# Performance work log

Measured on AMD Instinct MI355X. Metric: run time of the kernel, lower is better.

## Reference

```python
import jax, jax.numpy as jnp
import numpy as np

N_NODES = 50000
N_EDGES = 600000
D = 128
DROP_P = 0.5


def setup_inputs() -> dict:
    key = jax.random.key(0)
    k1, k2, k3, k4, k5, k6 = jax.random.split(key, 6)
    x = jax.random.normal(k1, (N_NODES, D), dtype=jnp.float32)
    W = jax.random.normal(k2, (D, D), dtype=jnp.float32) * (1.0 / np.sqrt(D))
    b = jax.random.normal(k3, (D,), dtype=jnp.float32) * 0.01
    mask_u = jax.random.uniform(k4, (N_NODES, D), dtype=jnp.float32)
    src = jax.random.randint(k5, (N_EDGES,), 0, N_NODES, dtype=jnp.int64)
    dst = jax.random.randint(k6, (N_EDGES,), 0, N_NODES, dtype=jnp.int64)
    return {"x": x, "W": W, "b": b, "mask_u": mask_u, "src": src, "dst": dst}


def reference(x, W, b, mask_u, src, dst):
    n_nodes = x.shape[0]
    # linear + relu (nn.Linear stores weight as [out, in]; here W is [out, in])
    h = jax.nn.relu(jnp.einsum('nd,od->no', x, W) + b)
    # inverted dropout with precomputed uniform noise (train mode, p=0.5)
    keep = (mask_u >= DROP_P).astype(h.dtype)
    h = h * keep * (1.0 / (1.0 - DROP_P))
    # message passing: msg = h[src], reduce = sum over incoming edges per dst
    msgs = jnp.take(h, src, axis=0)            # [E, D] gather
    out = jax.ops.segment_sum(msgs, dst, num_segments=n_nodes)  # [N, D]
    return out
```

## Files before the change

kernel.cpp:

```cpp
#include <hip/hip_runtime.h>

#define D 128
#define TILE_N 32
#define HPITCH 132
#define CAP 48
#define SPILL_MAX 8192

typedef __attribute__((ext_vector_type(8))) short  short8;
typedef __attribute__((ext_vector_type(4))) float  f32x4;

__device__ inline unsigned short f32_to_bf16(float f) {
    unsigned int u = __float_as_uint(f);
    unsigned int r = (u + 0x7FFFu + ((u >> 16) & 1u)) >> 16;
    return (unsigned short)r;
}
__device__ inline float bf16_to_f32(unsigned short s) {
    return __uint_as_float(((unsigned int)s) << 16);
}
__device__ inline short8 pack_bf16x8(float4 a, float4 b) {
    short8 u;
    u[0] = (short)f32_to_bf16(a.x); u[1] = (short)f32_to_bf16(a.y);
    u[2] = (short)f32_to_bf16(a.z); u[3] = (short)f32_to_bf16(a.w);
    u[4] = (short)f32_to_bf16(b.x); u[5] = (short)f32_to_bf16(b.y);
    u[6] = (short)f32_to_bf16(b.z); u[7] = (short)f32_to_bf16(b.w);
    return u;
}

__global__ __launch_bounds__(256) void prep_kernel(
    const float* __restrict__ W, unsigned short* __restrict__ Wb,
    int* __restrict__ cnt, int n_nodes, int* __restrict__ spill_cnt)
{
    const int tid = blockIdx.x * 256 + threadIdx.x;
    if (tid < (D * D) / 8) {
        float4 v0 = *(const float4*)&W[tid * 8];
        float4 v1 = *(const float4*)&W[tid * 8 + 4];
        *(short8*)&Wb[tid * 8] = pack_bf16x8(v0, v1);
    }
    if (cnt && tid < n_nodes) cnt[tid] = 0;
    if (spill_cnt && tid == 0) *spill_cnt = 0;
}

__global__ __launch_bounds__(256, 8) void gemm_mfma_kernel(
    const float* __restrict__ x, const unsigned short* __restrict__ Wb,
    const float* __restrict__ bias, const float* __restrict__ mask_u,
    unsigned short* __restrict__ h, int n_nodes,
    const int* __restrict__ src, const int* __restrict__ dst, int n_edges,
    int* __restrict__ cnt, int* __restrict__ bucket,
    int* __restrict__ spill_cnt, int* __restrict__ spill)
{
    __shared__ unsigned short ht[TILE_N * HPITCH];
    const int t    = threadIdx.x;
    const int lane = t & 63;
    const int w    = t >> 6;
    const int ws   = w >> 1;
    const int cs   = w & 1;
    const int fr   = lane & 15;
    const int fg   = lane >> 4;

    const int n0 = blockIdx.x * TILE_N;

    const int e0 = blockIdx.x * 256 + t;
    int e_dst = 0, e_src = 0;
    const bool has_e0 = (e0 < n_edges);
    if (has_e0) { e_dst = dst[e0]; e_src = src[e0]; }

    int arow = n0 + 16 * ws + fr;
    if (arow >= n_nodes) arow = n_nodes - 1;
    const float* xrow = x + (size_t)arow * D;
    float4 xa[4][2];
    #pragma unroll
    for (int s = 0; s < 4; ++s) {
        xa[s][0] = *(const float4*)&xrow[s * 32 + fg * 8];
        xa[s][1] = *(const float4*)&xrow[s * 32 + fg * 8 + 4];
    }

    float4 mk[2][2];
    int en_node[2];
    #pragma unroll
    for (int it = 0; it < 2; ++it) {
        const int idx = it * 256 + t;
        const int row = idx >> 4;
        const int cg  = idx & 15;
        int node = n0 + row;
        en_node[it] = node;
        if (node >= n_nodes) node = n_nodes - 1;
        const size_t off = (size_t)node * D + cg * 8;
        mk[it][0] = *(const float4*)&mask_u[off];
        mk[it][1] = *(const float4*)&mask_u[off + 4];
    }

    float bs[4];
    #pragma unroll
    for (int c = 0; c < 4; ++c) bs[c] = bias[64 * cs + 16 * c + fr];

    f32x4 acc[4];
    #pragma unroll
    for (int c = 0; c < 4; ++c) acc[c] = (f32x4){0.f, 0.f, 0.f, 0.f};

    #pragma unroll
    for (int s = 0; s < 4; ++s) {
        short8 a = pack_bf16x8(xa[s][0], xa[s][1]);
        #pragma unroll
        for (int c = 0; c < 4; ++c) {
            short8 b = *(const short8*)&Wb[(64 * cs + 16 * c + fr) * D + s * 32 + fg * 8];
            acc[c] = __builtin_amdgcn_mfma_f32_16x16x32_bf16(a, b, acc[c], 0, 0, 0);
        }
    }

    #pragma unroll
    for (int c = 0; c < 4; ++c) {
        const int col = 64 * cs + 16 * c + fr;
        #pragma unroll
        for (int r = 0; r < 4; ++r) {
            const int rl = 16 * ws + fg * 4 + r;
            float v = fmaxf(acc[c][r] + bs[c], 0.f);
            ht[rl * HPITCH + col] = f32_to_bf16(v);
        }
    }
    __syncthreads();

    if (has_e0) {
        int pos = atomicAdd(&cnt[e_dst], 1);
        if (pos < CAP) {
            bucket[e_dst * CAP + pos] = e_src;
        } else {
            int k = atomicAdd(spill_cnt, 1);
            if (k < SPILL_MAX) { spill[2 * k] = e_dst; spill[2 * k + 1] = e_src; }
        }
    }
    const int stride = gridDim.x * 256;
    for (int i = e0 + stride; i < n_edges; i += stride) {
        int dd  = dst[i];
        int ss  = src[i];
        int pos = atomicAdd(&cnt[dd], 1);
        if (pos < CAP) {
            bucket[dd * CAP + pos] = ss;
        } else {
            int k = atomicAdd(spill_cnt, 1);
            if (k < SPILL_MAX) { spill[2 * k] = dd; spill[2 * k + 1] = ss; }
        }
    }

    #pragma unroll
    for (int it = 0; it < 2; ++it) {
        const int idx = it * 256 + t;
        const int row = idx >> 4;
        const int cg  = idx & 15;
        if (en_node[it] < n_nodes) {
            short8 hv = *(const short8*)&ht[row * HPITCH + cg * 8];
            const size_t off = (size_t)en_node[it] * D + cg * 8;
            short8 o;
            #pragma unroll
            for (int j = 0; j < 8; ++j) {
                float m = (j < 4) ? ((const float*)&mk[it][0])[j]
                                  : ((const float*)&mk[it][1])[j - 4];
                float v = bf16_to_f32((unsigned short)hv[j]) * 2.f;
                o[j] = (m >= 0.5f) ? (short)f32_to_bf16(v) : (short)0;
            }
            *(short8*)&h[off] = o;
        }
    }
}

__global__ __launch_bounds__(256) void gather_reduce_kernel(
    const unsigned short* __restrict__ h, const int* __restrict__ cnt,
    const int* __restrict__ bucket, float* __restrict__ out, int n_nodes)
{
    const int t = threadIdx.x;
    const int node = blockIdx.x * 16 + (t >> 4);
    if (node >= n_nodes) return;
    const int cb = (t & 15) * 8;
    int deg = cnt[node];
    if (deg > CAP) deg = CAP;
    const int* b = bucket + (size_t)node * CAP;

    float acc[8];
    #pragma unroll
    for (int j = 0; j < 8; ++j) acc[j] = 0.f;

    int i = 0;
    for (; i + 3 < deg; i += 4) {
        int s0 = b[i], s1 = b[i + 1], s2 = b[i + 2], s3 = b[i + 3];
        short8 v0 = *(const short8*)&h[(size_t)s0 * D + cb];
        short8 v1 = *(const short8*)&h[(size_t)s1 * D + cb];
        short8 v2 = *(const short8*)&h[(size_t)s2 * D + cb];
        short8 v3 = *(const short8*)&h[(size_t)s3 * D + cb];
        #pragma unroll
        for (int j = 0; j < 8; ++j)
            acc[j] += (bf16_to_f32((unsigned short)v0[j]) +
                       bf16_to_f32((unsigned short)v1[j])) +
                      (bf16_to_f32((unsigned short)v2[j]) +
                       bf16_to_f32((unsigned short)v3[j]));
    }
    for (; i < deg; ++i) {
        int s0 = b[i];
        short8 v0 = *(const short8*)&h[(size_t)s0 * D + cb];
        #pragma unroll
        for (int j = 0; j < 8; ++j) acc[j] += bf16_to_f32((unsigned short)v0[j]);
    }

    f32x4 o0 = (f32x4){acc[0], acc[1], acc[2], acc[3]};
    f32x4 o1 = (f32x4){acc[4], acc[5], acc[6], acc[7]};
    __builtin_nontemporal_store(o0, (f32x4*)&out[(size_t)node * D + cb]);
    __builtin_nontemporal_store(o1, (f32x4*)&out[(size_t)node * D + cb + 4]);
}

__global__ __launch_bounds__(256) void spill_apply_kernel(
    const unsigned short* __restrict__ h, const int* __restrict__ spill_cnt,
    const int* __restrict__ spill, float* __restrict__ out)
{
    int n = *spill_cnt;
    if (n > SPILL_MAX) n = SPILL_MAX;
    for (int e = threadIdx.x; e < n; e += 256) {
        int dd = spill[2 * e], ss = spill[2 * e + 1];
        for (int j = 0; j < D; ++j)
            atomicAdd(&out[(size_t)dd * D + j],
                      bf16_to_f32(h[(size_t)ss * D + j]));
    }
}

__global__ __launch_bounds__(256) void zero_kernel(int* __restrict__ p, int n)
{
    int i = blockIdx.x * 256 + threadIdx.x;
    if (i < n) p[i] = 0;
}

__global__ __launch_bounds__(256) void scatter_atomic_kernel(
    const unsigned short* __restrict__ h, const int* __restrict__ src,
    const int* __restrict__ dst, float* __restrict__ out, int n_edges)
{
    const int t = threadIdx.x;
    const int e = blockIdx.x * 16 + (t >> 4);
    if (e >= n_edges) return;
    const int cb = (t & 15) * 8;
    const int s  = src[e];
    const int dd = dst[e];
    short8 v = *(const short8*)&h[(size_t)s * D + cb];
    float* o = &out[(size_t)dd * D + cb];
    #pragma unroll
    for (int j = 0; j < 8; ++j) atomicAdd(o + j, bf16_to_f32((unsigned short)v[j]));
}

extern "C" void kernel_launch(void* const* d_in, const int* in_sizes, int n_in,
                              void* d_out, int out_size, void* d_ws, size_t ws_size,
                              hipStream_t stream) {
    const float* x      = (const float*)d_in[0];
    const float* W      = (const float*)d_in[1];
    const float* bias   = (const float*)d_in[2];
    const float* mask_u = (const float*)d_in[3];
    const int*   src    = (const int*)d_in[4];
    const int*   dst    = (const int*)d_in[5];
    float* out = (float*)d_out;

    const int n_nodes = in_sizes[0] / D;
    const int n_edges = in_sizes[4];
    const int n_tiles = (n_nodes + TILE_N - 1) / TILE_N;

    unsigned short* Wb = (unsigned short*)d_ws;
    const size_t wb_bytes = (size_t)D * D * sizeof(unsigned short);
    unsigned short* h  = (unsigned short*)((char*)d_ws + wb_bytes);
    const size_t h_bytes = (size_t)n_nodes * D * sizeof(unsigned short);
    int* cnt       = (int*)((char*)d_ws + wb_bytes + h_bytes);
    int* spill_cnt = cnt + n_nodes;
    int* spill     = spill_cnt + 1;
    int* bucket    = spill + 2 * SPILL_MAX;
    const size_t needed = wb_bytes + h_bytes +
        ((size_t)n_nodes + 1 + 2 * SPILL_MAX + (size_t)n_nodes * CAP) * sizeof(int);

    const int pbk = ((n_nodes > 2048 ? n_nodes : 2048) + 255) / 256;

    if (ws_size >= needed) {
        prep_kernel<<<pbk, 256, 0, stream>>>(W, Wb, cnt, n_nodes, spill_cnt);
        gemm_mfma_kernel<<<n_tiles, 256, 0, stream>>>(
            x, Wb, bias, mask_u, h, n_nodes,
            src, dst, n_edges, cnt, bucket, spill_cnt, spill);
        gather_reduce_kernel<<<(n_nodes + 15) / 16, 256, 0, stream>>>(
            h, cnt, bucket, out, n_nodes);
        spill_apply_kernel<<<1, 256, 0, stream>>>(h, spill_cnt, spill, out);
    } else {
        prep_kernel<<<8, 256, 0, stream>>>(W, Wb, nullptr, 0, nullptr);
        gemm_mfma_kernel<<<n_tiles, 256, 0, stream>>>(
            x, Wb, bias, mask_u, h, n_nodes,
            nullptr, nullptr, 0, nullptr, nullptr, nullptr, nullptr);
        zero_kernel<<<(out_size + 255) / 256, 256, 0, stream>>>((int*)d_out, out_size);
        scatter_atomic_kernel<<<(n_edges + 15) / 16, 256, 0, stream>>>(
            h, src, dst, out, n_edges);
    }
}
```

Before: 79.64 us.

## Pre-convert x to bf16 and mask to bitmask in prep; halve GEMM tile

The prep kernel now also converts x to bf16 and packs the dropout mask into one bit per element, using a grid-stride loop over 2048 blocks. The GEMM kernel then reads the compact bf16 rows and mask bytes, with TILE_N halved to 16 and each wave computing 32 output columns. This gives more blocks and a smaller per-thread working set. The cost is an extra full pass that reads x and mask_u and writes the intermediate buffers. The low-workspace fallback is replaced by a simple scalar GEMM kernel.

```diff
diff --git a/kernel.cpp b/kernel.cpp
--- a/kernel.cpp
+++ b/kernel.cpp
@@ -1,7 +1,7 @@
 #include <hip/hip_runtime.h>
 
 #define D 128
-#define TILE_N 32
+#define TILE_N 16
 #define HPITCH 132
 #define CAP 48
 #define SPILL_MAX 8192
@@ -28,21 +28,41 @@
 
 __global__ __launch_bounds__(256) void prep_kernel(
     const float* __restrict__ W, unsigned short* __restrict__ Wb,
+    const float* __restrict__ x, unsigned short* __restrict__ xb,
+    const float* __restrict__ mask_u, unsigned char* __restrict__ mbits,
     int* __restrict__ cnt, int n_nodes, int* __restrict__ spill_cnt)
 {
     const int tid = blockIdx.x * 256 + threadIdx.x;
-    if (tid < (D * D) / 8) {
-        float4 v0 = *(const float4*)&W[tid * 8];
-        float4 v1 = *(const float4*)&W[tid * 8 + 4];
-        *(short8*)&Wb[tid * 8] = pack_bf16x8(v0, v1);
-    }
-    if (cnt && tid < n_nodes) cnt[tid] = 0;
-    if (spill_cnt && tid == 0) *spill_cnt = 0;
+    const int nth = gridDim.x * 256;
+
+    for (int i = tid; i < (D * D) / 8; i += nth) {
+        float4 v0 = *(const float4*)&W[i * 8];
+        float4 v1 = *(const float4*)&W[i * 8 + 4];
+        *(short8*)&Wb[i * 8] = pack_bf16x8(v0, v1);
+    }
+    const int nx8 = n_nodes * (D / 8);
+    for (int i = tid; i < nx8; i += nth) {
+        float4 v0 = *(const float4*)&x[(size_t)i * 8];
+        float4 v1 = *(const float4*)&x[(size_t)i * 8 + 4];
+        *(short8*)&xb[(size_t)i * 8] = pack_bf16x8(v0, v1);
+    }
+    for (int i = tid; i < nx8; i += nth) {
+        float4 m0 = *(const float4*)&mask_u[(size_t)i * 8];
+        float4 m1 = *(const float4*)&mask_u[(size_t)i * 8 + 4];
+        unsigned b = 0;
+        b |= (m0.x >= 0.5f) ? 1u : 0u;   b |= (m0.y >= 0.5f) ? 2u : 0u;
+        b |= (m0.z >= 0.5f) ? 4u : 0u;   b |= (m0.w >= 0.5f) ? 8u : 0u;
+        b |= (m1.x >= 0.5f) ? 16u : 0u;  b |= (m1.y >= 0.5f) ? 32u : 0u;
+        b |= (m1.z >= 0.5f) ? 64u : 0u;  b |= (m1.w >= 0.5f) ? 128u : 0u;
+        mbits[i] = (unsigned char)b;
+    }
+    for (int i = tid; i < n_nodes; i += nth) cnt[i] = 0;
+    if (tid == 0 && spill_cnt) *spill_cnt = 0;
 }
 
 __global__ __launch_bounds__(256, 8) void gemm_mfma_kernel(
-    const float* __restrict__ x, const unsigned short* __restrict__ Wb,
-    const float* __restrict__ bias, const float* __restrict__ mask_u,
+    const unsigned short* __restrict__ xb, const unsigned short* __restrict__ Wb,
+    const float* __restrict__ bias, const unsigned char* __restrict__ mbits,
     unsigned short* __restrict__ h, int n_nodes,
     const int* __restrict__ src, const int* __restrict__ dst, int n_edges,
     int* __restrict__ cnt, int* __restrict__ bucket,
@@ -52,11 +72,8 @@
     const int t    = threadIdx.x;
     const int lane = t & 63;
     const int w    = t >> 6;
-    const int ws   = w >> 1;
-    const int cs   = w & 1;
     const int fr   = lane & 15;
     const int fg   = lane >> 4;
-
     const int n0 = blockIdx.x * TILE_N;
 
     const int e0 = blockIdx.x * 256 + t;
@@ -64,58 +81,45 @@
     const bool has_e0 = (e0 < n_edges);
     if (has_e0) { e_dst = dst[e0]; e_src = src[e0]; }
 
-    int arow = n0 + 16 * ws + fr;
+    const int prow = t >> 4;
+    const int pcg  = t & 15;
+    const int pnode = n0 + prow;
+    const bool pvalid = (pnode < n_nodes);
+    unsigned mbyte = 0;
+    if (pvalid) mbyte = mbits[pnode * 16 + pcg];
+
+    int arow = n0 + fr;
     if (arow >= n_nodes) arow = n_nodes - 1;
-    const float* xrow = x + (size_t)arow * D;
-    float4 xa[4][2];
+    const unsigned short* xr = xb + (size_t)arow * D;
+    short8 a0 = *(const short8*)&xr[ 0 + fg * 8];
+    short8 a1 = *(const short8*)&xr[32 + fg * 8];
+    short8 a2 = *(const short8*)&xr[64 + fg * 8];
+    short8 a3 = *(const short8*)&xr[96 + fg * 8];
+
+    const float bs0 = bias[32 * w + fr];
+    const float bs1 = bias[32 * w + 16 + fr];
+
+    const unsigned short* wb0 = Wb + (size_t)(32 * w + fr) * D;
+    const unsigned short* wb1 = Wb + (size_t)(32 * w + 16 + fr) * D;
+
+    f32x4 acc0 = (f32x4){0.f, 0.f, 0.f, 0.f};
+    f32x4 acc1 = (f32x4){0.f, 0.f, 0.f, 0.f};
     #pragma unroll
     for (int s = 0; s < 4; ++s) {
-        xa[s][0] = *(const float4*)&xrow[s * 32 + fg * 8];
-        xa[s][1] = *(const float4*)&xrow[s * 32 + fg * 8 + 4];
-    }
-
-    float4 mk[2][2];
-    int en_node[2];
+        short8 a = (s == 0) ? a0 : (s == 1) ? a1 : (s == 2) ? a2 : a3;
+        short8 b0 = *(const short8*)&wb0[s * 32 + fg * 8];
+        short8 b1 = *(const short8*)&wb1[s * 32 + fg * 8];
+        acc0 = __builtin_amdgcn_mfma_f32_16x16x32_bf16(a, b0, acc0, 0, 0, 0);
+        acc1 = __builtin_amdgcn_mfma_f32_16x16x32_bf16(a, b1, acc1, 0, 0, 0);
+    }
+
     #pragma unroll
-    for (int it = 0; it < 2; ++it) {
-        const int idx = it * 256 + t;
-        const int row = idx >> 4;
-        const int cg  = idx & 15;
-        int node = n0 + row;
-        en_node[it] = node;
-        if (node >= n_nodes) node = n_nodes - 1;
-        const size_t off = (size_t)node * D + cg * 8;
-        mk[it][0] = *(const float4*)&mask_u[off];
-        mk[it][1] = *(const float4*)&mask_u[off + 4];
-    }
-
-    float bs[4];
-    #pragma unroll
-    for (int c = 0; c < 4; ++c) bs[c] = bias[64 * cs + 16 * c + fr];
-
-    f32x4 acc[4];
-    #pragma unroll
-    for (int c = 0; c < 4; ++c) acc[c] = (f32x4){0.f, 0.f, 0.f, 0.f};
-
-    #pragma unroll
-    for (int s = 0; s < 4; ++s) {
-        short8 a = pack_bf16x8(xa[s][0], xa[s][1]);
-        #pragma unroll
-        for (int c = 0; c < 4; ++c) {
-            short8 b = *(const short8*)&Wb[(64 * cs + 16 * c + fr) * D + s * 32 + fg * 8];
-            acc[c] = __builtin_amdgcn_mfma_f32_16x16x32_bf16(a, b, acc[c], 0, 0, 0);
-        }
-    }
-
-    #pragma unroll
-    for (int c = 0; c < 4; ++c) {
-        const int col = 64 * cs + 16 * c + fr;
-        #pragma unroll
-        for (int r = 0; r < 4; ++r) {
-            const int rl = 16 * ws + fg * 4 + r;
-            float v = fmaxf(acc[c][r] + bs[c], 0.f);
-            ht[rl * HPITCH + col] = f32_to_bf16(v);
-        }
+    for (int r = 0; r < 4; ++r) {
+        const int rl = fg * 4 + r;
+        float v0 = fmaxf(acc0[r] + bs0, 0.f);
+        float v1 = fmaxf(acc1[r] + bs1, 0.f);
+        ht[rl * HPITCH + 32 * w + fr]      = f32_to_bf16(v0);
+        ht[rl * HPITCH + 32 * w + 16 + fr] = f32_to_bf16(v1);
     }
     __syncthreads();
 
@@ -141,24 +145,15 @@
         }
     }
 
-    #pragma unroll
-    for (int it = 0; it < 2; ++it) {
-        const int idx = it * 256 + t;
-        const int row = idx >> 4;
-        const int cg  = idx & 15;
-        if (en_node[it] < n_nodes) {
-            short8 hv = *(const short8*)&ht[row * HPITCH + cg * 8];
-            const size_t off = (size_t)en_node[it] * D + cg * 8;
-            short8 o;
-            #pragma unroll
-            for (int j = 0; j < 8; ++j) {
-                float m = (j < 4) ? ((const float*)&mk[it][0])[j]
-                                  : ((const float*)&mk[it][1])[j - 4];
-                float v = bf16_to_f32((unsigned short)hv[j]) * 2.f;
-                o[j] = (m >= 0.5f) ? (short)f32_to_bf16(v) : (short)0;
-            }
-            *(short8*)&h[off] = o;
+    if (pvalid) {
+        short8 hv = *(const short8*)&ht[prow * HPITCH + pcg * 8];
+        short8 o;
+        #pragma unroll
+        for (int j = 0; j < 8; ++j) {
+            float v = bf16_to_f32((unsigned short)hv[j]) * 2.f;
+            o[j] = ((mbyte >> j) & 1u) ? (short)f32_to_bf16(v) : (short)0;
         }
+        *(short8*)&h[(size_t)pnode * D + pcg * 8] = o;
     }
 }
 
@@ -225,6 +220,27 @@
     if (i < n) p[i] = 0;
 }
 
+__global__ __launch_bounds__(256) void gemm_fb_kernel(
+    const float* __restrict__ x, const float* __restrict__ W,
+    const float* __restrict__ bias, const float* __restrict__ mask_u,
+    unsigned short* __restrict__ h, int n_nodes)
+{
+    int tid = blockIdx.x * 256 + threadIdx.x;
+    if (tid >= n_nodes * 16) return;
+    int node = tid >> 4, cg = tid & 15;
+    for (int c = 0; c < 8; ++c) {
+        int col = cg * 8 + c;
+        float s = bias[col];
+        for (int k = 0; k < D; ++k)
+            s += bf16_to_f32(f32_to_bf16(x[(size_t)node * D + k])) *
+                 bf16_to_f32(f32_to_bf16(W[(size_t)col * D + k]));
+        s = fmaxf(s, 0.f);
+        float m = mask_u[(size_t)node * D + col];
+        s *= (m >= 0.5f) ? 2.f : 0.f;
+        h[(size_t)node * D + col] = f32_to_bf16(s);
+    }
+}
+
 __global__ __launch_bounds__(256) void scatter_atomic_kernel(
     const unsigned short* __restrict__ h, const int* __restrict__ src,
     const int* __restrict__ dst, float* __restrict__ out, int n_edges)
@@ -256,34 +272,36 @@
     const int n_edges = in_sizes[4];
     const int n_tiles = (n_nodes + TILE_N - 1) / TILE_N;
 
+    const size_t wb_bytes = (size_t)D * D * sizeof(unsigned short);
+    const size_t xb_bytes = (size_t)n_nodes * D * sizeof(unsigned short);
+    const size_t h_bytes  = (size_t)n_nodes * D * sizeof(unsigned short);
     unsigned short* Wb = (unsigned short*)d_ws;
-    const size_t wb_bytes = (size_t)D * D * sizeof(unsigned short);
-    unsigned short* h  = (unsigned short*)((char*)d_ws + wb_bytes);
-    const size_t h_bytes = (size_t)n_nodes * D * sizeof(unsigned short);
-    int* cnt       = (int*)((char*)d_ws + wb_bytes + h_bytes);
+    unsigned short* xb = (unsigned short*)((char*)d_ws + wb_bytes);
+    unsigned short* h  = (unsigned short*)((char*)d_ws + wb_bytes + xb_bytes);
+    int* cnt       = (int*)((char*)d_ws + wb_bytes + xb_bytes + h_bytes);
     int* spill_cnt = cnt + n_nodes;
     int* spill     = spill_cnt + 1;
     int* bucket    = spill + 2 * SPILL_MAX;
-    const size_t needed = wb_bytes + h_bytes +
-        ((size_t)n_nodes + 1 + 2 * SPILL_MAX + (size_t)n_nodes * CAP) * sizeof(int);
-
-    const int pbk = ((n_nodes > 2048 ? n_nodes : 2048) + 255) / 256;
+    unsigned char* mbits = (unsigned char*)(bucket + (size_t)n_nodes * CAP);
+    const size_t needed = wb_bytes + xb_bytes + h_bytes +
+        ((size_t)n_nodes + 1 + 2 * SPILL_MAX + (size_t)n_nodes * CAP) * sizeof(int) +
+        (size_t)n_nodes * 16;
 
     if (ws_size >= needed) {
-        prep_kernel<<<pbk, 256, 0, stream>>>(W, Wb, cnt, n_nodes, spill_cnt);
+        prep_kernel<<<2048, 256, 0, stream>>>(
+            W, Wb, x, xb, mask_u, mbits, cnt, n_nodes, spill_cnt);
         gemm_mfma_kernel<<<n_tiles, 256, 0, stream>>>(
-            x, Wb, bias, mask_u, h, n_nodes,
+            xb, Wb, bias, mbits, h, n_nodes,
             src, dst, n_edges, cnt, bucket, spill_cnt, spill);
         gather_reduce_kernel<<<(n_nodes + 15) / 16, 256, 0, stream>>>(
             h, cnt, bucket, out, n_nodes);
         spill_apply_kernel<<<1, 256, 0, stream>>>(h, spill_cnt, spill, out);
     } else {
-        prep_kernel<<<8, 256, 0, stream>>>(W, Wb, nullptr, 0, nullptr);
-        gemm_mfma_kernel<<<n_tiles, 256, 0, stream>>>(
-            x, Wb, bias, mask_u, h, n_nodes,
-            nullptr, nullptr, 0, nullptr, nullptr, nullptr, nullptr);
+        unsigned short* hf = (unsigned short*)d_ws;
+        gemm_fb_kernel<<<(n_nodes * 16 + 255) / 256, 256, 0, stream>>>(
+            x, W, bias, mask_u, hf, n_nodes);
         zero_kernel<<<(out_size + 255) / 256, 256, 0, stream>>>((int*)d_out, out_size);
         scatter_atomic_kernel<<<(n_edges + 15) / 16, 256, 0, stream>>>(
-            h, src, dst, out, n_edges);
-    }
-}
+            hf, src, dst, out, n_edges);
+    }
+}
```

Result: slower. 84.07 us (+5.6%).
